# Optimization experiments

Measured on AMD Instinct MI355X. Metric: run time of the kernel, lower is better.

The kernel has to match this reference:

```python
import jax, jax.numpy as jnp
import numpy as np

B, L = 2048, 4096


def setup_inputs() -> dict:
    key = jax.random.key(0)
    k1, k2, k3 = jax.random.split(key, 3)
    j = jax.random.normal(k1, (1,), dtype=jnp.float32)
    b = jax.random.normal(k2, (2,), dtype=jnp.float32)
    observations = jax.random.randint(k3, (B, L), 0, 2, dtype=jnp.int64)
    return {"j": j, "b": b, "observations": observations}


def reference(j, b, observations):
    dt = j.dtype
    values = jnp.array([-0.5, 0.5], dtype=dt)           # 2 latent states
    pairs = values[:, None] * values[None, :]            # [2,2] outer product
    psi = j * pairs                                      # pairwise max-plus potential [2,2]
    # unary potentials: phi[b_idx, i, s] = b[obs[b_idx, i]] * values[s]
    phi = b[observations][..., None] * values            # [B, L, 2]
    zeros2 = jnp.zeros((2,), dtype=dt)

    def step(msg, phi_i):
        # max-plus message update: max over source state s of phi[s] + psi[s,t] + msg[s]
        new = jnp.max(phi_i[:, None] + psi + msg[:, None], axis=0)
        return new, new

    def per_seq(phi_seq):  # phi_seq: [L, 2]
        # forward messages: column 0 is zeros, column i+1 is msg from step i (i = 0..L-2)
        _, f = jax.lax.scan(step, zeros2, phi_seq[:-1])
        fwd = jnp.concatenate([zeros2[None], f], axis=0)       # [L, 2]
        # backward messages: iterate i = L-1 down to 1; msg from step i lands at column i-1
        _, bk = jax.lax.scan(step, zeros2, phi_seq[:0:-1])
        bwd = jnp.concatenate([bk[::-1], zeros2[None]], axis=0)  # [L, 2]
        return (phi_seq + fwd + bwd).T                          # [2, L]

    return jax.vmap(per_seq)(phi)  # [B, 2, L]
```

## Files before the change

kernel.cpp:

```cpp
#include <hip/hip_runtime.h>
#include <math.h>

#define L_SEQ 4096
#define NT 512
#define CHUNK 8
#define NW (NT/64)

typedef float f2 __attribute__((ext_vector_type(2)));

__device__ __forceinline__ f2 mkf2(float a, float b) { f2 r; r.x = a; r.y = b; return r; }
__device__ __forceinline__ f2 max2(f2 a, f2 b) { return mkf2(fmaxf(a.x, b.x), fmaxf(a.y, b.y)); }
__device__ __forceinline__ float hmax(f2 v) { return fmaxf(v.x, v.y); }

struct M2 { f2 r0, r1; };

__device__ __forceinline__ M2 mpc(const M2& A, const M2& B) {
  M2 C;
  C.r0 = max2(mkf2(A.r0.x, A.r0.x) + B.r0, mkf2(A.r0.y, A.r0.y) + B.r1);
  C.r1 = max2(mkf2(A.r1.x, A.r1.x) + B.r0, mkf2(A.r1.y, A.r1.y) + B.r1);
  return C;
}
__device__ __forceinline__ f2 mapply(f2 v, const M2& M) {
  return max2(mkf2(v.x, v.x) + M.r0, mkf2(v.y, v.y) + M.r1);
}
__device__ __forceinline__ f2 colmax(const M2& M) { return max2(M.r0, M.r1); }

__device__ __forceinline__ M2 ld4(float4 v) { M2 M; M.r0 = mkf2(v.x, v.y); M.r1 = mkf2(v.z, v.w); return M; }
__device__ __forceinline__ float4 st4(const M2& M) { return make_float4(M.r0.x, M.r0.y, M.r1.x, M.r1.y); }

template <int CTRL>
__device__ __forceinline__ float dppf(float x) {
  return __int_as_float(__builtin_amdgcn_update_dpp(
      0, __float_as_int(x), CTRL, 0xf, 0xf, true));
}
template <int CTRL>
__device__ __forceinline__ f2 dpp2(f2 x) { return mkf2(dppf<CTRL>(x.x), dppf<CTRL>(x.y)); }
template <int CTRL>
__device__ __forceinline__ M2 dpp_fetch(const M2& x) {
  M2 r; r.r0 = dpp2<CTRL>(x.r0); r.r1 = dpp2<CTRL>(x.r1); return r;
}
__device__ __forceinline__ float rdl(float x, int l) {
  return __int_as_float(__builtin_amdgcn_readlane(__float_as_int(x), l));
}

__global__ __launch_bounds__(NT, 8) void chain_fb_kernel(
    const float* __restrict__ jp, const float* __restrict__ bp,
    const int* __restrict__ obs, float* __restrict__ out) {
  __shared__ float4 T4s[16];
  __shared__ f2 T8r0[256], T8r1[256];
  __shared__ float4 wtf[NW];
  __shared__ float4 wtbr[NW];

  const int t = threadIdx.x;
  const int lane = t & 63;
  const int w = t >> 6;
  const long b = blockIdx.x;

  const float P   = 0.25f * jp[0];
  const float hb0 = 0.5f * bp[0];
  const float hb1 = 0.5f * bp[1];

  const int4* rowp = (const int4*)(obs + b * L_SEQ + (long)t * CHUNK);
  int4 q0 = rowp[0], q1 = rowp[1];

  if (t < 16) {
    float u0 = (t & 1) ? hb1 : hb0;
    M2 Tt; Tt.r0 = mkf2(P - u0, -u0 - P); Tt.r1 = mkf2(u0 - P, u0 + P);
    #pragma unroll
    for (int k = 1; k < 4; ++k) {
      float uk = ((t >> k) & 1) ? hb1 : hb0;
      M2 Ek; Ek.r0 = mkf2(P - uk, -uk - P); Ek.r1 = mkf2(uk - P, uk + P);
      Tt = mpc(Tt, Ek);
    }
    T4s[t] = st4(Tt);
  }
  __syncthreads();
  if (t < 256) {
    M2 M = mpc(ld4(T4s[t & 15]), ld4(T4s[(t >> 4) & 15]));
    T8r0[t] = M.r0; T8r1[t] = M.r1;
  }
  const unsigned m =
      (unsigned)(q0.x & 1)       | (unsigned)(q0.y & 1) << 1 |
      (unsigned)(q0.z & 1) << 2  | (unsigned)(q0.w & 1) << 3 |
      (unsigned)(q1.x & 1) << 4  | (unsigned)(q1.y & 1) << 5 |
      (unsigned)(q1.z & 1) << 6  | (unsigned)(q1.w & 1) << 7;
  __syncthreads();

  const unsigned mrev = (unsigned)__shfl((int)m, 63 - lane);
  const unsigned r = __brev(mrev) >> 24;
  M2 T;  T.r0  = T8r0[m]; T.r1  = T8r1[m];
  M2 Rv; Rv.r0 = T8r0[r]; Rv.r1 = T8r1[r];

  {
    M2 f, g;
    f = dpp_fetch<0x111>(T); g = dpp_fetch<0x111>(Rv);
    if ((lane & 15) >= 1) { T = mpc(f, T); Rv = mpc(g, Rv); }
    f = dpp_fetch<0x112>(T); g = dpp_fetch<0x112>(Rv);
    if ((lane & 15) >= 2) { T = mpc(f, T); Rv = mpc(g, Rv); }
    f = dpp_fetch<0x114>(T); g = dpp_fetch<0x114>(Rv);
    if ((lane & 15) >= 4) { T = mpc(f, T); Rv = mpc(g, Rv); }
    f = dpp_fetch<0x118>(T); g = dpp_fetch<0x118>(Rv);
    if ((lane & 15) >= 8) { T = mpc(f, T); Rv = mpc(g, Rv); }
    f = dpp_fetch<0x142>(T); g = dpp_fetch<0x142>(Rv);
    if (lane & 16)        { T = mpc(f, T); Rv = mpc(g, Rv); }
    f = dpp_fetch<0x143>(T); g = dpp_fetch<0x143>(Rv);
    if (lane >= 32)       { T = mpc(f, T); Rv = mpc(g, Rv); }
  }
  if (lane == 63) { wtf[w] = st4(T); wtbr[7 - w] = st4(Rv); }

  __syncthreads();

  M2 Xf = ld4(wtf[lane & 7]);
  M2 Xb = ld4(wtbr[lane & 7]);
  {
    M2 f, g;
    f = dpp_fetch<0x111>(Xf); g = dpp_fetch<0x111>(Xb);
    if ((lane & 15) >= 1) { Xf = mpc(f, Xf); Xb = mpc(g, Xb); }
    f = dpp_fetch<0x112>(Xf); g = dpp_fetch<0x112>(Xb);
    if ((lane & 15) >= 2) { Xf = mpc(f, Xf); Xb = mpc(g, Xb); }
    f = dpp_fetch<0x114>(Xf); g = dpp_fetch<0x114>(Xb);
    if ((lane & 15) >= 4) { Xf = mpc(f, Xf); Xb = mpc(g, Xb); }
  }
  const f2 Vf = colmax(Xf);
  const f2 Vb = colmax(Xb);

  f2 v, vb;
  if (w > 0) v = mkf2(rdl(Vf.x, w - 1), rdl(Vf.y, w - 1));
  else       v = mkf2(0.f, 0.f);
  if (w < 7) vb = mkf2(rdl(Vb.x, 6 - w), rdl(Vb.y, 6 - w));
  else       vb = mkf2(0.f, 0.f);

  f2 wv  = mapply(v,  T);
  f2 wvb = mapply(vb, Rv);
  f2 fm  = dpp2<0x138>(wv);
  f2 bmv = dpp2<0x138>(wvb);
  if (lane == 0) { fm = v; bmv = vb; }
  f2 bm = mkf2(__shfl(bmv.x, 63 - lane), __shfl(bmv.y, 63 - lane));

  f2 uv[CHUNK];
  #pragma unroll
  for (int e = 0; e < CHUNK; ++e) {
    float u = ((m >> e) & 1) ? hb1 : hb0;
    uv[e] = mkf2(-u, u);
  }

  const f2 pp = mkf2(P, -P), pm = mkf2(-P, P);
  const long base = (long)t * CHUNK;
  float* r0 = out + b * (2L * L_SEQ) + base;
  float* r1 = r0 + L_SEQ;

  f2 o[CHUNK];
  #pragma unroll
  for (int e = 0; e < CHUNK; ++e) {
    f2 xy = fm + uv[e];
    o[e] = xy;
    fm = mkf2(hmax(xy + pp), hmax(xy + pm));
  }
  #pragma unroll
  for (int e = CHUNK - 1; e >= 0; --e) {
    o[e] += bm;
    f2 xy = bm + uv[e];
    bm = mkf2(hmax(xy + pp), hmax(xy + pm));
    if (e == 4) {
      ((float4*)r0)[1] = make_float4(o[4].x, o[5].x, o[6].x, o[7].x);
      ((float4*)r1)[1] = make_float4(o[4].y, o[5].y, o[6].y, o[7].y);
    }
  }
  ((float4*)r0)[0] = make_float4(o[0].x, o[1].x, o[2].x, o[3].x);
  ((float4*)r1)[0] = make_float4(o[0].y, o[1].y, o[2].y, o[3].y);
}

extern "C" void kernel_launch(void* const* d_in, const int* in_sizes, int n_in,
                              void* d_out, int out_size, void* d_ws, size_t ws_size,
                              hipStream_t stream) {
  const float* jp  = (const float*)d_in[0];
  const float* bp  = (const float*)d_in[1];
  const int*   obs = (const int*)d_in[2];
  float* out = (float*)d_out;
  const int B = in_sizes[2] / L_SEQ;
  chain_fb_kernel<<<B, NT, 0, stream>>>(jp, bp, obs, out);
}
```

Measured before the change: 23.23 us.

## Use 1024 threads with 4-element chunks and drop the 8-step table build

Doubles threads per block to 1024 and halves each thread's chunk to 4 positions. The 256-entry 8-step transfer table and its extra barrier and build phase are replaced by a 16-entry 4-step table. The cross-wave scan grows to 16 waves with one more DPP level. This gives more parallelism per sequence and less serial work per thread, at the cost of larger blocks, lower occupancy limits under launch_bounds(1024,8), and more scan overhead.

```diff
diff --git a/kernel.cpp b/kernel.cpp
--- a/kernel.cpp
+++ b/kernel.cpp
@@ -2,8 +2,8 @@
 #include <math.h>
 
 #define L_SEQ 4096
-#define NT 512
-#define CHUNK 8
+#define NT 1024
+#define CHUNK 4
 #define NW (NT/64)
 
 typedef float f2 __attribute__((ext_vector_type(2)));
@@ -46,8 +46,7 @@
 __global__ __launch_bounds__(NT, 8) void chain_fb_kernel(
     const float* __restrict__ jp, const float* __restrict__ bp,
     const int* __restrict__ obs, float* __restrict__ out) {
-  __shared__ float4 T4s[16];
-  __shared__ f2 T8r0[256], T8r1[256];
+  __shared__ f2 T4r0[16], T4r1[16];
   __shared__ float4 wtf[NW];
   __shared__ float4 wtbr[NW];
 
@@ -60,8 +59,7 @@
   const float hb0 = 0.5f * bp[0];
   const float hb1 = 0.5f * bp[1];
 
-  const int4* rowp = (const int4*)(obs + b * L_SEQ + (long)t * CHUNK);
-  int4 q0 = rowp[0], q1 = rowp[1];
+  const int4 q0 = *(const int4*)(obs + b * L_SEQ + (long)t * CHUNK);
 
   if (t < 16) {
     float u0 = (t & 1) ? hb1 : hb0;
@@ -72,24 +70,17 @@
       M2 Ek; Ek.r0 = mkf2(P - uk, -uk - P); Ek.r1 = mkf2(uk - P, uk + P);
       Tt = mpc(Tt, Ek);
     }
-    T4s[t] = st4(Tt);
-  }
-  __syncthreads();
-  if (t < 256) {
-    M2 M = mpc(ld4(T4s[t & 15]), ld4(T4s[(t >> 4) & 15]));
-    T8r0[t] = M.r0; T8r1[t] = M.r1;
+    T4r0[t] = Tt.r0; T4r1[t] = Tt.r1;
   }
   const unsigned m =
-      (unsigned)(q0.x & 1)       | (unsigned)(q0.y & 1) << 1 |
-      (unsigned)(q0.z & 1) << 2  | (unsigned)(q0.w & 1) << 3 |
-      (unsigned)(q1.x & 1) << 4  | (unsigned)(q1.y & 1) << 5 |
-      (unsigned)(q1.z & 1) << 6  | (unsigned)(q1.w & 1) << 7;
+      (unsigned)(q0.x & 1)      | (unsigned)(q0.y & 1) << 1 |
+      (unsigned)(q0.z & 1) << 2 | (unsigned)(q0.w & 1) << 3;
   __syncthreads();
 
   const unsigned mrev = (unsigned)__shfl((int)m, 63 - lane);
-  const unsigned r = __brev(mrev) >> 24;
-  M2 T;  T.r0  = T8r0[m]; T.r1  = T8r1[m];
-  M2 Rv; Rv.r0 = T8r0[r]; Rv.r1 = T8r1[r];
+  const unsigned r = __brev(mrev) >> 28;
+  M2 T;  T.r0  = T4r0[m]; T.r1  = T4r1[m];
+  M2 Rv; Rv.r0 = T4r0[r]; Rv.r1 = T4r1[r];
 
   {
     M2 f, g;
@@ -106,12 +97,12 @@
     f = dpp_fetch<0x143>(T); g = dpp_fetch<0x143>(Rv);
     if (lane >= 32)       { T = mpc(f, T); Rv = mpc(g, Rv); }
   }
-  if (lane == 63) { wtf[w] = st4(T); wtbr[7 - w] = st4(Rv); }
+  if (lane == 63) { wtf[w] = st4(T); wtbr[NW - 1 - w] = st4(Rv); }
 
   __syncthreads();
 
-  M2 Xf = ld4(wtf[lane & 7]);
-  M2 Xb = ld4(wtbr[lane & 7]);
+  M2 Xf = ld4(wtf[lane & 15]);
+  M2 Xb = ld4(wtbr[lane & 15]);
   {
     M2 f, g;
     f = dpp_fetch<0x111>(Xf); g = dpp_fetch<0x111>(Xb);
@@ -120,15 +111,17 @@
     if ((lane & 15) >= 2) { Xf = mpc(f, Xf); Xb = mpc(g, Xb); }
     f = dpp_fetch<0x114>(Xf); g = dpp_fetch<0x114>(Xb);
     if ((lane & 15) >= 4) { Xf = mpc(f, Xf); Xb = mpc(g, Xb); }
+    f = dpp_fetch<0x118>(Xf); g = dpp_fetch<0x118>(Xb);
+    if ((lane & 15) >= 8) { Xf = mpc(f, Xf); Xb = mpc(g, Xb); }
   }
   const f2 Vf = colmax(Xf);
   const f2 Vb = colmax(Xb);
 
   f2 v, vb;
-  if (w > 0) v = mkf2(rdl(Vf.x, w - 1), rdl(Vf.y, w - 1));
-  else       v = mkf2(0.f, 0.f);
-  if (w < 7) vb = mkf2(rdl(Vb.x, 6 - w), rdl(Vb.y, 6 - w));
-  else       vb = mkf2(0.f, 0.f);
+  if (w > 0)      v  = mkf2(rdl(Vf.x, w - 1), rdl(Vf.y, w - 1));
+  else            v  = mkf2(0.f, 0.f);
+  if (w < NW - 1) vb = mkf2(rdl(Vb.x, NW - 2 - w), rdl(Vb.y, NW - 2 - w));
+  else            vb = mkf2(0.f, 0.f);
 
   f2 wv  = mapply(v,  T);
   f2 wvb = mapply(vb, Rv);
@@ -145,9 +138,6 @@
   }
 
   const f2 pp = mkf2(P, -P), pm = mkf2(-P, P);
-  const long base = (long)t * CHUNK;
-  float* r0 = out + b * (2L * L_SEQ) + base;
-  float* r1 = r0 + L_SEQ;
 
   f2 o[CHUNK];
   #pragma unroll
@@ -161,13 +151,13 @@
     o[e] += bm;
     f2 xy = bm + uv[e];
     bm = mkf2(hmax(xy + pp), hmax(xy + pm));
-    if (e == 4) {
-      ((float4*)r0)[1] = make_float4(o[4].x, o[5].x, o[6].x, o[7].x);
-      ((float4*)r1)[1] = make_float4(o[4].y, o[5].y, o[6].y, o[7].y);
-    }
   }
-  ((float4*)r0)[0] = make_float4(o[0].x, o[1].x, o[2].x, o[3].x);
-  ((float4*)r1)[0] = make_float4(o[0].y, o[1].y, o[2].y, o[3].y);
+
+  const long base = (long)t * CHUNK;
+  float* r0 = out + b * (2L * L_SEQ) + base;
+  float* r1 = r0 + L_SEQ;
+  *(float4*)r0 = make_float4(o[0].x, o[1].x, o[2].x, o[3].x);
+  *(float4*)r1 = make_float4(o[0].y, o[1].y, o[2].y, o[3].y);
 }
 
 extern "C" void kernel_launch(void* const* d_in, const int* in_sizes, int n_in,
```

After: 32.28 us. +38.9%, slower.

## Map one sequence per wavefront with 64-element chunks, removing cross-wave scan

Applied to the files above, without the earlier changes.

Each wavefront now processes a whole sequence, with each lane handling 64 positions as eight 8-element groups. Lanes compose per-group max-plus transfer matrices from the shared lookup table before a wave-level DPP scan. This removes the cross-wave shared-memory exchange and the second block barrier. It costs much more serial work and register use per lane, fewer threads per block (256 vs 512), and strided 64-element per-lane global accesses that may coalesce poorly.

```diff
diff --git a/kernel.cpp b/kernel.cpp
--- a/kernel.cpp
+++ b/kernel.cpp
@@ -2,9 +2,10 @@
 #include <math.h>
 
 #define L_SEQ 4096
-#define NT 512
-#define CHUNK 8
-#define NW (NT/64)
+#define NT 256
+#define SPW 4
+#define NG 8
+#define CHUNK 64
 
 typedef float f2 __attribute__((ext_vector_type(2)));
 
@@ -24,7 +25,6 @@
   return max2(mkf2(v.x, v.x) + M.r0, mkf2(v.y, v.y) + M.r1);
 }
 __device__ __forceinline__ f2 colmax(const M2& M) { return max2(M.r0, M.r1); }
-
 __device__ __forceinline__ M2 ld4(float4 v) { M2 M; M.r0 = mkf2(v.x, v.y); M.r1 = mkf2(v.z, v.w); return M; }
 __device__ __forceinline__ float4 st4(const M2& M) { return make_float4(M.r0.x, M.r0.y, M.r1.x, M.r1.y); }
 
@@ -39,29 +39,33 @@
 __device__ __forceinline__ M2 dpp_fetch(const M2& x) {
   M2 r; r.r0 = dpp2<CTRL>(x.r0); r.r1 = dpp2<CTRL>(x.r1); return r;
 }
-__device__ __forceinline__ float rdl(float x, int l) {
-  return __int_as_float(__builtin_amdgcn_readlane(__float_as_int(x), l));
+
+__device__ __forceinline__ unsigned pack8(const int4& a, const int4& b) {
+  return (unsigned)a.x        | (unsigned)a.y << 1 |
+         (unsigned)a.z << 2   | (unsigned)a.w << 3 |
+         (unsigned)b.x << 4   | (unsigned)b.y << 5 |
+         (unsigned)b.z << 6   | (unsigned)b.w << 7;
 }
 
-__global__ __launch_bounds__(NT, 8) void chain_fb_kernel(
+__global__ __launch_bounds__(NT, 2) void chain_fb_kernel(
     const float* __restrict__ jp, const float* __restrict__ bp,
     const int* __restrict__ obs, float* __restrict__ out) {
   __shared__ float4 T4s[16];
   __shared__ f2 T8r0[256], T8r1[256];
-  __shared__ float4 wtf[NW];
-  __shared__ float4 wtbr[NW];
 
   const int t = threadIdx.x;
   const int lane = t & 63;
   const int w = t >> 6;
-  const long b = blockIdx.x;
+  const long seq = (long)blockIdx.x * SPW + w;
 
   const float P   = 0.25f * jp[0];
   const float hb0 = 0.5f * bp[0];
   const float hb1 = 0.5f * bp[1];
 
-  const int4* rowp = (const int4*)(obs + b * L_SEQ + (long)t * CHUNK);
-  int4 q0 = rowp[0], q1 = rowp[1];
+  const int4* rowp = (const int4*)(obs + seq * L_SEQ + (long)lane * CHUNK);
+  int4 q[16];
+  #pragma unroll
+  for (int i = 0; i < 16; ++i) q[i] = rowp[i];
 
   if (t < 16) {
     float u0 = (t & 1) ? hb1 : hb0;
@@ -75,21 +79,32 @@
     T4s[t] = st4(Tt);
   }
   __syncthreads();
-  if (t < 256) {
+  {
     M2 M = mpc(ld4(T4s[t & 15]), ld4(T4s[(t >> 4) & 15]));
     T8r0[t] = M.r0; T8r1[t] = M.r1;
   }
-  const unsigned m =
-      (unsigned)(q0.x & 1)       | (unsigned)(q0.y & 1) << 1 |
-      (unsigned)(q0.z & 1) << 2  | (unsigned)(q0.w & 1) << 3 |
-      (unsigned)(q1.x & 1) << 4  | (unsigned)(q1.y & 1) << 5 |
-      (unsigned)(q1.z & 1) << 6  | (unsigned)(q1.w & 1) << 7;
+  const unsigned mlo = pack8(q[0], q[1])        | pack8(q[2], q[3]) << 8 |
+                       pack8(q[4], q[5]) << 16  | pack8(q[6], q[7]) << 24;
+  const unsigned mhi = pack8(q[8], q[9])        | pack8(q[10], q[11]) << 8 |
+                       pack8(q[12], q[13]) << 16 | pack8(q[14], q[15]) << 24;
   __syncthreads();
 
-  const unsigned mrev = (unsigned)__shfl((int)m, 63 - lane);
-  const unsigned r = __brev(mrev) >> 24;
-  M2 T;  T.r0  = T8r0[m]; T.r1  = T8r1[m];
-  M2 Rv; Rv.r0 = T8r0[r]; Rv.r1 = T8r1[r];
+  const unsigned rlo_me = __brev(mhi), rhi_me = __brev(mlo);
+  const unsigned olo = (unsigned)__shfl((int)mlo, 63 - lane);
+  const unsigned ohi = (unsigned)__shfl((int)mhi, 63 - lane);
+  const unsigned rlo_o = __brev(ohi), rhi_o = __brev(olo);
+
+  M2 T;  T.r0  = T8r0[mlo & 255];   T.r1  = T8r1[mlo & 255];
+  M2 Rv; Rv.r0 = T8r0[rlo_o & 255]; Rv.r1 = T8r1[rlo_o & 255];
+  #pragma unroll
+  for (int g = 1; g < NG; ++g) {
+    const unsigned pf = (g < 4 ? mlo >> (8 * g)   : mhi >> (8 * (g - 4))) & 255;
+    const unsigned pb = (g < 4 ? rlo_o >> (8 * g) : rhi_o >> (8 * (g - 4))) & 255;
+    M2 Mf; Mf.r0 = T8r0[pf]; Mf.r1 = T8r1[pf];
+    M2 Mb; Mb.r0 = T8r0[pb]; Mb.r1 = T8r1[pb];
+    T  = mpc(T,  Mf);
+    Rv = mpc(Rv, Mb);
+  }
 
   {
     M2 f, g;
@@ -106,68 +121,54 @@
     f = dpp_fetch<0x143>(T); g = dpp_fetch<0x143>(Rv);
     if (lane >= 32)       { T = mpc(f, T); Rv = mpc(g, Rv); }
   }
-  if (lane == 63) { wtf[w] = st4(T); wtbr[7 - w] = st4(Rv); }
 
-  __syncthreads();
-
-  M2 Xf = ld4(wtf[lane & 7]);
-  M2 Xb = ld4(wtbr[lane & 7]);
-  {
-    M2 f, g;
-    f = dpp_fetch<0x111>(Xf); g = dpp_fetch<0x111>(Xb);
-    if ((lane & 15) >= 1) { Xf = mpc(f, Xf); Xb = mpc(g, Xb); }
-    f = dpp_fetch<0x112>(Xf); g = dpp_fetch<0x112>(Xb);
-    if ((lane & 15) >= 2) { Xf = mpc(f, Xf); Xb = mpc(g, Xb); }
-    f = dpp_fetch<0x114>(Xf); g = dpp_fetch<0x114>(Xb);
-    if ((lane & 15) >= 4) { Xf = mpc(f, Xf); Xb = mpc(g, Xb); }
-  }
-  const f2 Vf = colmax(Xf);
-  const f2 Vb = colmax(Xb);
-
-  f2 v, vb;
-  if (w > 0) v = mkf2(rdl(Vf.x, w - 1), rdl(Vf.y, w - 1));
-  else       v = mkf2(0.f, 0.f);
-  if (w < 7) vb = mkf2(rdl(Vb.x, 6 - w), rdl(Vb.y, 6 - w));
-  else       vb = mkf2(0.f, 0.f);
-
-  f2 wv  = mapply(v,  T);
-  f2 wvb = mapply(vb, Rv);
+  f2 wv  = colmax(T);
+  f2 wvb = colmax(Rv);
   f2 fm  = dpp2<0x138>(wv);
   f2 bmv = dpp2<0x138>(wvb);
-  if (lane == 0) { fm = v; bmv = vb; }
+  if (lane == 0) { fm = mkf2(0.f, 0.f); bmv = mkf2(0.f, 0.f); }
   f2 bm = mkf2(__shfl(bmv.x, 63 - lane), __shfl(bmv.y, 63 - lane));
 
-  f2 uv[CHUNK];
+  f2 B[NG];
+  B[NG - 1] = bm;
   #pragma unroll
-  for (int e = 0; e < CHUNK; ++e) {
-    float u = ((m >> e) & 1) ? hb1 : hb0;
-    uv[e] = mkf2(-u, u);
+  for (int k = 0; k < NG - 1; ++k) {
+    const unsigned pb = (k < 4 ? rlo_me >> (8 * k) : rhi_me >> (8 * (k - 4))) & 255;
+    M2 Mb; Mb.r0 = T8r0[pb]; Mb.r1 = T8r1[pb];
+    B[NG - 2 - k] = mapply(B[NG - 1 - k], Mb);
   }
 
   const f2 pp = mkf2(P, -P), pm = mkf2(-P, P);
-  const long base = (long)t * CHUNK;
-  float* r0 = out + b * (2L * L_SEQ) + base;
+  const f2 uvl = mkf2(-hb0, hb0), uvh = mkf2(-hb1, hb1);
+  float* r0 = out + seq * (2L * L_SEQ) + (long)lane * CHUNK;
   float* r1 = r0 + L_SEQ;
 
-  f2 o[CHUNK];
   #pragma unroll
-  for (int e = 0; e < CHUNK; ++e) {
-    f2 xy = fm + uv[e];
-    o[e] = xy;
-    fm = mkf2(hmax(xy + pp), hmax(xy + pm));
+  for (int g = 0; g < NG; ++g) {
+    const unsigned grp = (g < 4 ? mlo >> (8 * g) : mhi >> (8 * (g - 4))) & 255;
+    f2 uv[8];
+    #pragma unroll
+    for (int k = 0; k < 8; ++k) uv[k] = ((grp >> k) & 1) ? uvh : uvl;
+
+    f2 be[8];
+    be[7] = B[g];
+    #pragma unroll
+    for (int k = 6; k >= 0; --k) {
+      f2 xy = be[k + 1] + uv[k + 1];
+      be[k] = mkf2(hmax(xy + pp), hmax(xy + pm));
+    }
+    f2 o[8];
+    #pragma unroll
+    for (int k = 0; k < 8; ++k) {
+      f2 xy = fm + uv[k];
+      o[k] = xy + be[k];
+      fm = mkf2(hmax(xy + pp), hmax(xy + pm));
+    }
+    ((float4*)(r0 + g * 8))[0] = make_float4(o[0].x, o[1].x, o[2].x, o[3].x);
+    ((float4*)(r0 + g * 8))[1] = make_float4(o[4].x, o[5].x, o[6].x, o[7].x);
+    ((float4*)(r1 + g * 8))[0] = make_float4(o[0].y, o[1].y, o[2].y, o[3].y);
+    ((float4*)(r1 + g * 8))[1] = make_float4(o[4].y, o[5].y, o[6].y, o[7].y);
   }
-  #pragma unroll
-  for (int e = CHUNK - 1; e >= 0; --e) {
-    o[e] += bm;
-    f2 xy = bm + uv[e];
-    bm = mkf2(hmax(xy + pp), hmax(xy + pm));
-    if (e == 4) {
-      ((float4*)r0)[1] = make_float4(o[4].x, o[5].x, o[6].x, o[7].x);
-      ((float4*)r1)[1] = make_float4(o[4].y, o[5].y, o[6].y, o[7].y);
-    }
-  }
-  ((float4*)r0)[0] = make_float4(o[0].x, o[1].x, o[2].x, o[3].x);
-  ((float4*)r1)[0] = make_float4(o[0].y, o[1].y, o[2].y, o[3].y);
 }
 
 extern "C" void kernel_launch(void* const* d_in, const int* in_sizes, int n_in,
@@ -178,5 +179,5 @@
   const int*   obs = (const int*)d_in[2];
   float* out = (float*)d_out;
   const int B = in_sizes[2] / L_SEQ;
-  chain_fb_kernel<<<B, NT, 0, stream>>>(jp, bp, obs, out);
+  chain_fb_kernel<<<B / SPW, NT, 0, stream>>>(jp, bp, obs, out);
 }
```

After: 69.50 us. +199.1%, slower.
